# Kernel optimization log

Hardware: AMD Instinct MI355X
Metric: run time of the kernel (lower is better)

## Reference

```python
import jax, jax.numpy as jnp
import numpy as np

B, N, C, H = 4, 4096, 1024, 16
EPS = 1e-6


def setup_inputs() -> dict:
    key = jax.random.key(0)
    k1, k2, k3 = jax.random.split(key, 3)
    x = jax.random.normal(k1, (B, N, C), dtype=jnp.float32)
    qkv_w = jax.random.normal(k2, (3 * C, C), dtype=jnp.float32) * 0.02
    qkv_b = jnp.zeros((3 * C,), dtype=jnp.float32)
    proj_w = jax.random.normal(k3, (C, C), dtype=jnp.float32) * 0.02
    proj_b = jnp.zeros((C,), dtype=jnp.float32)
    return {"x": x, "qkv_w": qkv_w, "qkv_b": qkv_b, "proj_w": proj_w, "proj_b": proj_b}


def reference(x, qkv_w, qkv_b, proj_w, proj_b):
    b, n, c = x.shape
    d = c // H
    # qkv projection: (B,N,3C) -> (3,B,H,N,D)
    qkv = x @ qkv_w.T + qkv_b
    qkv = qkv.reshape(b, n, 3, H, d).transpose(2, 0, 3, 1, 4)
    q, k, v = qkv[0], qkv[1], qkv[2]
    # non-negative kernel
    q = jax.nn.sigmoid(q)
    k = jax.nn.sigmoid(k)
    # sink / source normalization (all per (B,H,N))
    k_sum = k.sum(axis=2)                                   # (B,H,D)
    sink_incoming = 1.0 / jnp.sum((q + EPS) * (k_sum[:, :, None, :] + EPS), axis=-1)
    q_sum = q.sum(axis=2)                                   # (B,H,D)
    source_outgoing = 1.0 / jnp.sum((k + EPS) * (q_sum[:, :, None, :] + EPS), axis=-1)
    k_so_sum = (k * source_outgoing[..., None]).sum(axis=2, keepdims=True)  # (B,H,1,D)
    conserved_sink = jnp.sum((q + EPS) * (k_so_sum + EPS), axis=-1) + EPS   # (B,H,N)
    q_si_sum = (q * sink_incoming[..., None]).sum(axis=2, keepdims=True)    # (B,H,1,D)
    conserved_source = jnp.sum((k + EPS) * (q_si_sum + EPS), axis=-1) + EPS # (B,H,N)
    conserved_source = jnp.clip(conserved_source, -1.0, 1.0)
    ratio = float(n) / float(n)  # q_len / k_len == 1 for self-attention
    sink_allocation = jax.nn.sigmoid(conserved_sink * ratio)               # (B,H,N)
    source_competition = jax.nn.softmax(conserved_source, axis=-1) * float(n)
    q_norm = q * sink_incoming[..., None]
    v_comp = v * source_competition[..., None]
    # linear-time attention: (B,H,D,D) then (B,H,N,D)
    kv = jnp.einsum('bhnd,bhnm->bhdm', k, v_comp)
    out = jnp.einsum('bhnd,bhdm->bhnm', q_norm, kv)
    out = out * sink_allocation[..., None]
    out = out.transpose(0, 2, 1, 3).reshape(b, n, c)
    out = out @ proj_w.T + proj_b
    # dropout is identity in eval mode
    return out
```

## Files before the change

kernel.cpp:

```cpp
#include <hip/hip_runtime.h>
#include <cstdint>
#include <cstddef>

#define EPSF 1e-6f

static constexpr int Bc  = 4;
static constexpr int Nc  = 4096;
static constexpr int Hc  = 16;
static constexpr int Dc  = 64;
static constexpr size_t HEADSZ = (size_t)64 * Nc * Dc;
static constexpr int Kd  = 1024;

typedef __attribute__((ext_vector_type(8))) short     s16x8;
typedef __attribute__((ext_vector_type(4))) float     f32x4;

__device__ __forceinline__ float sigmoid_f(float x) {
  return 1.0f / (1.0f + __expf(-x));
}

__device__ __forceinline__ unsigned short bf16_rne(float x) {
  unsigned int b = __float_as_uint(x);
  b += 0x7fffu + ((b >> 16) & 1u);
  return (unsigned short)(b >> 16);
}
__device__ __forceinline__ float bf16_to_f(unsigned short u) {
  return __uint_as_float(((unsigned int)u) << 16);
}
__device__ __forceinline__ void split_trunc(float x, unsigned short& h, unsigned short& l) {
  unsigned int b  = __float_as_uint(x);
  unsigned int hb = b & 0xffff0000u;
  h = (unsigned short)(hb >> 16);
  float res = x - __uint_as_float(hb);
  l = (unsigned short)(__float_as_uint(res) >> 16);
}

__device__ __forceinline__ void gl_lds16(const unsigned short* g, unsigned short* l) {
  __builtin_amdgcn_global_load_lds(
      (const __attribute__((address_space(1))) unsigned int*)(const void*)g,
      (__attribute__((address_space(3))) unsigned int*)(void*)l,
      16, 0, 0);
}

__global__ __launch_bounds__(256)
void split_kernel(const float* __restrict__ in, unsigned short* __restrict__ hi,
                  unsigned short* __restrict__ lo, int n4)
{
  int i = blockIdx.x * 256 + threadIdx.x;
  if (i >= n4) return;
  float4 v = ((const float4*)in)[i];
  ushort4 h, l;
  h.x = bf16_rne(v.x); l.x = bf16_rne(v.x - bf16_to_f(h.x));
  h.y = bf16_rne(v.y); l.y = bf16_rne(v.y - bf16_to_f(h.y));
  h.z = bf16_rne(v.z); l.z = bf16_rne(v.z - bf16_to_f(h.z));
  h.w = bf16_rne(v.w); l.w = bf16_rne(v.w - bf16_to_f(h.w));
  ((ushort4*)hi)[i] = h;
  ((ushort4*)lo)[i] = l;
}

template <int MODE>
__global__ __launch_bounds__(256)
void gemm_mfma(const unsigned short* __restrict__ Ah_g, const unsigned short* __restrict__ Al_g,
               const unsigned short* __restrict__ Wh_g, const unsigned short* __restrict__ Wl_g,
               const float* __restrict__ bias,
               float* __restrict__ out0, float* __restrict__ out1, float* __restrict__ out2,
               float* __restrict__ qsum_g, float* __restrict__ ksum_g)
{
  __shared__ unsigned short Ahs[128][32];
  __shared__ unsigned short Als[128][32];
  __shared__ unsigned short Whs[128][32];
  __shared__ unsigned short Wls[128][32];

  const int bid = blockIdx.x;
  const int xcd = bid & 7;
  const int idx = bid >> 3;
  int bx, by;
  if constexpr (MODE == 0) {
    bx = idx / 3;
    by = xcd * 3 + idx % 3;
  } else {
    bx = xcd * 16 + (idx >> 3);
    by = idx & 7;
  }

  const int t    = threadIdx.x;
  const int lane = t & 63;
  const int wid  = t >> 6;
  const int wr   = wid >> 1, wc = wid & 1;
  const int r16  = lane & 15, g = lane >> 4;
  const int m0   = bx * 128;
  const int r0   = by * 128;

  const int wrow = wid * 32;
  const int wl_r = lane >> 2;
  const int wl_c = (lane & 3) * 8;
  unsigned short* AhsF = &Ahs[0][0];
  unsigned short* AlsF = &Als[0][0];
  unsigned short* WhsF = &Whs[0][0];
  unsigned short* WlsF = &Wls[0][0];

  f32x4 acc[4][4];
#pragma unroll
  for (int i = 0; i < 4; ++i)
#pragma unroll
    for (int j = 0; j < 4; ++j) acc[i][j] = (f32x4){0.f, 0.f, 0.f, 0.f};

  for (int kt = 0; kt < Kd; kt += 32) {
    __syncthreads();
#pragma unroll
    for (int j = 0; j < 2; ++j) {
      const size_t ga  = (size_t)(m0 + wrow + j*16 + wl_r) * Kd + kt + wl_c;
      const size_t gw  = (size_t)(r0 + wrow + j*16 + wl_r) * Kd + kt + wl_c;
      const int    lof = wid * 1024 + j * 512;
      gl_lds16(Ah_g + ga, AhsF + lof);
      gl_lds16(Al_g + ga, AlsF + lof);
      gl_lds16(Wh_g + gw, WhsF + lof);
      gl_lds16(Wl_g + gw, WlsF + lof);
    }
    __syncthreads();

    s16x8 fah[4], fal[4], fbh[4], fbl[4];
#pragma unroll
    for (int i = 0; i < 4; ++i) {
      const int row = wr * 64 + i * 16 + r16;
      fah[i] = *(const s16x8*)&Ahs[row][g * 8];
      fal[i] = *(const s16x8*)&Als[row][g * 8];
    }
#pragma unroll
    for (int j = 0; j < 4; ++j) {
      const int row = wc * 64 + j * 16 + r16;
      fbh[j] = *(const s16x8*)&Whs[row][g * 8];
      fbl[j] = *(const s16x8*)&Wls[row][g * 8];
    }
#pragma unroll
    for (int i = 0; i < 4; ++i) {
#pragma unroll
      for (int j = 0; j < 4; ++j) {
        acc[i][j] = __builtin_amdgcn_mfma_f32_16x16x32_bf16(fah[i], fbh[j], acc[i][j], 0, 0, 0);
        acc[i][j] = __builtin_amdgcn_mfma_f32_16x16x32_bf16(fah[i], fbl[j], acc[i][j], 0, 0, 0);
        acc[i][j] = __builtin_amdgcn_mfma_f32_16x16x32_bf16(fal[i], fbh[j], acc[i][j], 0, 0, 0);
      }
    }
  }

#pragma unroll
  for (int nj = 0; nj < 4; ++nj) {
    const int colb = r0 + wc * 64 + nj * 16;
    const float bj = bias[colb + r16];
    if constexpr (MODE == 0) {
      const int tsel = colb >> 10;
      const int h    = (colb & 1023) >> 6;
      const int d    = (colb & 63) + r16;
      float* dst = (tsel == 0) ? out0 : (tsel == 1) ? out1 : out2;
      const bool sig = (tsel < 2);
      float ssum = 0.f;
#pragma unroll
      for (int mi = 0; mi < 4; ++mi) {
#pragma unroll
        for (int rg = 0; rg < 4; ++rg) {
          const int m = m0 + wr * 64 + mi * 16 + g * 4 + rg;
          float xv = acc[mi][nj][rg] + bj;
          if (sig) { xv = sigmoid_f(xv); ssum += xv; }
          const int b = m >> 12, n = m & 4095;
          dst[((size_t)(b * Hc + h) * Nc + n) * Dc + d] = xv;
        }
      }
      if (sig) {
        ssum += __shfl_xor(ssum, 16);
        ssum += __shfl_xor(ssum, 32);
        if (g == 0) {
          const int b = (m0 + wr * 64) >> 12;
          float* sdst = (tsel == 0) ? qsum_g : ksum_g;
          atomicAdd(&sdst[(b * Hc + h) * 64 + d], ssum);
        }
      }
    } else {
#pragma unroll
      for (int mi = 0; mi < 4; ++mi) {
#pragma unroll
        for (int rg = 0; rg < 4; ++rg) {
          const int m = m0 + wr * 64 + mi * 16 + g * 4 + rg;
          out0[(size_t)m * 1024 + colb + r16] = acc[mi][nj][rg] + bj;
        }
      }
    }
  }
}

__global__ __launch_bounds__(256)
void siso_kernel(const float* __restrict__ qb, const float* __restrict__ kb,
                 const float* __restrict__ q_sum, const float* __restrict__ k_sum,
                 float* __restrict__ si,
                 float* __restrict__ q_si_sum, float* __restrict__ k_so_sum)
{
  const int bh = blockIdx.x;
  const int t = threadIdx.x, lane = t & 63, w = t >> 6;
  const int c = lane & 15, r = lane >> 4;
  float4 ksd = *(const float4*)&k_sum[bh*64 + c*4];
  float4 qsd = *(const float4*)&q_sum[bh*64 + c*4];
  ksd.x += EPSF; ksd.y += EPSF; ksd.z += EPSF; ksd.w += EPSF;
  qsd.x += EPSF; qsd.y += EPSF; qsd.z += EPSF; qsd.w += EPSF;
  float4 qsi_p = {0,0,0,0}, kso_p = {0,0,0,0};
  const size_t rowbase = (size_t)bh * Nc;
  const int n00 = blockIdx.y * 256 + w * 64;
  for (int i = 0; i < 16; ++i) {
    const int n = n00 + i*4 + r;
    const size_t off = (rowbase + n) * Dc + c*4;
    float4 qv = *(const float4*)&qb[off];
    float4 kv = *(const float4*)&kb[off];
    float s1 = (qv.x+EPSF)*ksd.x + (qv.y+EPSF)*ksd.y + (qv.z+EPSF)*ksd.z + (qv.w+EPSF)*ksd.w;
    float s2 = (kv.x+EPSF)*qsd.x + (kv.y+EPSF)*qsd.y + (kv.z+EPSF)*qsd.z + (kv.w+EPSF)*qsd.w;
#pragma unroll
    for (int o = 1; o < 16; o <<= 1) {
      s1 += __shfl_xor(s1, o);
      s2 += __shfl_xor(s2, o);
    }
    const float si_n = 1.f / s1;
    const float so_n = 1.f / s2;
    if (c == 0) si[rowbase + n] = si_n;
    qsi_p.x = __builtin_fmaf(qv.x, si_n, qsi_p.x);
    qsi_p.y = __builtin_fmaf(qv.y, si_n, qsi_p.y);
    qsi_p.z = __builtin_fmaf(qv.z, si_n, qsi_p.z);
    qsi_p.w = __builtin_fmaf(qv.w, si_n, qsi_p.w);
    kso_p.x = __builtin_fmaf(kv.x, so_n, kso_p.x);
    kso_p.y = __builtin_fmaf(kv.y, so_n, kso_p.y);
    kso_p.z = __builtin_fmaf(kv.z, so_n, kso_p.z);
    kso_p.w = __builtin_fmaf(kv.w, so_n, kso_p.w);
  }
#pragma unroll
  for (int o = 16; o < 64; o <<= 1) {
    qsi_p.x += __shfl_xor(qsi_p.x, o); qsi_p.y += __shfl_xor(qsi_p.y, o);
    qsi_p.z += __shfl_xor(qsi_p.z, o); qsi_p.w += __shfl_xor(qsi_p.w, o);
    kso_p.x += __shfl_xor(kso_p.x, o); kso_p.y += __shfl_xor(kso_p.y, o);
    kso_p.z += __shfl_xor(kso_p.z, o); kso_p.w += __shfl_xor(kso_p.w, o);
  }
  __shared__ float red[2][4][64];
  if (r == 0) {
    *(float4*)&red[0][w][c*4] = qsi_p;
    *(float4*)&red[1][w][c*4] = kso_p;
  }
  __syncthreads();
  if (t < 64) {
    atomicAdd(&q_si_sum[bh*64 + t], red[0][0][t]+red[0][1][t]+red[0][2][t]+red[0][3][t]);
  } else if (t < 128) {
    const int l = t - 64;
    atomicAdd(&k_so_sum[bh*64 + l], red[1][0][l]+red[1][1][l]+red[1][2][l]+red[1][3][l]);
  }
}

__global__ __launch_bounds__(256)
void conserved_kernel(const float* __restrict__ qb, const float* __restrict__ kb,
                      const float* __restrict__ q_si_sum, const float* __restrict__ k_so_sum,
                      const float* __restrict__ si,
                      float* __restrict__ qscale, float* __restrict__ sc_raw,
                      float* __restrict__ exp_sum)
{
  const int bh = blockIdx.x;
  const int t = threadIdx.x, lane = t & 63, w = t >> 6;
  const int c = lane & 15, r = lane >> 4;
  float4 ksod = *(const float4*)&k_so_sum[bh*64 + c*4];
  float4 qsid = *(const float4*)&q_si_sum[bh*64 + c*4];
  ksod.x += EPSF; ksod.y += EPSF; ksod.z += EPSF; ksod.w += EPSF;
  qsid.x += EPSF; qsid.y += EPSF; qsid.z += EPSF; qsid.w += EPSF;
  float ep = 0.f;
  const size_t rowbase = (size_t)bh * Nc;
  const int n00 = blockIdx.y * 256 + w * 64;
  for (int i = 0; i < 16; ++i) {
    const int n = n00 + i*4 + r;
    const size_t off = (rowbase + n) * Dc + c*4;
    float4 qv = *(const float4*)&qb[off];
    float4 kv = *(const float4*)&kb[off];
    float s1 = (qv.x+EPSF)*ksod.x + (qv.y+EPSF)*ksod.y + (qv.z+EPSF)*ksod.z + (qv.w+EPSF)*ksod.w;
    float s2 = (kv.x+EPSF)*qsid.x + (kv.y+EPSF)*qsid.y + (kv.z+EPSF)*qsid.z + (kv.w+EPSF)*qsid.w;
#pragma unroll
    for (int o = 1; o < 16; o <<= 1) {
      s1 += __shfl_xor(s1, o);
      s2 += __shfl_xor(s2, o);
    }
    if (c == 0) {
      const float sa = sigmoid_f(s1 + EPSF);
      float cs = s2 + EPSF;
      cs = fminf(fmaxf(cs, -1.f), 1.f);
      const float e = __expf(cs);
      qscale[rowbase + n] = sa * si[rowbase + n];
      sc_raw[rowbase + n] = e;
      ep += e;
    }
  }
  ep += __shfl_xor(ep, 16);
  ep += __shfl_xor(ep, 32);
  __shared__ float red[4];
  if (lane == 0) red[w] = ep;
  __syncthreads();
  if (t == 0) atomicAdd(&exp_sum[bh], red[0]+red[1]+red[2]+red[3]);
}

__global__ __launch_bounds__(256)
void kv_kernel(const float* __restrict__ kb, const float* __restrict__ vb,
               const float* __restrict__ sc_raw, const float* __restrict__ exp_sum,
               float* __restrict__ kvout)
{
  const int bh = blockIdx.x, ch = blockIdx.y;
  const int t = threadIdx.x;
  const int m = t & 63, dg = t >> 6;
  const float scl = (float)Nc / exp_sum[bh];
  __shared__ float ks[64][64];
  __shared__ float vs[64][64];
  float acc[16];
#pragma unroll
  for (int i = 0; i < 16; ++i) acc[i] = 0.f;

  for (int c0 = ch*256; c0 < ch*256 + 256; c0 += 64) {
    __syncthreads();
#pragma unroll
    for (int j = 0; j < 4; ++j) {
      const int f = t + 256*j;
      const int row = f >> 4, cb = (f & 15) * 4;
      const size_t gidx = ((size_t)bh*Nc + c0 + row) * Dc + cb;
      *(float4*)&ks[row][cb] = *(const float4*)&kb[gidx];
      float4 vv = *(const float4*)&vb[gidx];
      const float s = sc_raw[(size_t)bh*Nc + c0 + row] * scl;
      vv.x *= s; vv.y *= s; vv.z *= s; vv.w *= s;
      *(float4*)&vs[row][cb] = vv;
    }
    __syncthreads();
#pragma unroll 8
    for (int n = 0; n < 64; ++n) {
      const float vv = vs[n][m];
#pragma unroll
      for (int dd = 0; dd < 4; ++dd) {
        float4 kk = *(const float4*)&ks[n][dg*16 + dd*4];
        acc[dd*4+0] = __builtin_fmaf(kk.x, vv, acc[dd*4+0]);
        acc[dd*4+1] = __builtin_fmaf(kk.y, vv, acc[dd*4+1]);
        acc[dd*4+2] = __builtin_fmaf(kk.z, vv, acc[dd*4+2]);
        acc[dd*4+3] = __builtin_fmaf(kk.w, vv, acc[dd*4+3]);
      }
    }
  }
#pragma unroll
  for (int dd = 0; dd < 16; ++dd)
    atomicAdd(&kvout[(size_t)bh*4096 + (size_t)(dg*16 + dd)*64 + m], acc[dd]);
}

__global__ __launch_bounds__(256)
void out_kernel(const float* __restrict__ qb, const float* __restrict__ kvin,
                const float* __restrict__ qscale,
                unsigned short* __restrict__ attn_h, unsigned short* __restrict__ attn_l)
{
  const int bh = blockIdx.x, cy = blockIdx.y;
  const int t = threadIdx.x;
  const int c0 = cy * 64;
  __shared__ float kvs[64][68];
  __shared__ float qT[64][68];
  __shared__ float qsc[64];

#pragma unroll
  for (int j = 0; j < 4; ++j) {
    const int f = t + 256*j;
    const int d = f >> 4, cb = (f & 15) * 4;
    *(float4*)&kvs[d][cb] = *(const float4*)&kvin[(size_t)bh*4096 + (size_t)d*64 + cb];
  }
#pragma unroll
  for (int j = 0; j < 4; ++j) {
    const int f = t + 256*j;
    const int n = f >> 4, db = (f & 15) * 4;
    float4 qv = *(const float4*)&qb[((size_t)bh*Nc + c0 + n) * Dc + db];
    qT[db+0][n] = qv.x; qT[db+1][n] = qv.y; qT[db+2][n] = qv.z; qT[db+3][n] = qv.w;
  }
  if (t < 16) *(float4*)&qsc[t*4] = *(const float4*)&qscale[(size_t)bh*Nc + c0 + t*4];
  __syncthreads();

  const int ng = t & 15, mg = t >> 4;
  float acc[4][4];
#pragma unroll
  for (int i = 0; i < 4; ++i)
#pragma unroll
    for (int j = 0; j < 4; ++j) acc[i][j] = 0.f;

#pragma unroll 16
  for (int d = 0; d < 64; ++d) {
    float4 a = *(const float4*)&qT[d][ng*4];
    float4 b = *(const float4*)&kvs[d][mg*4];
    float av[4] = {a.x,a.y,a.z,a.w};
    float bv[4] = {b.x,b.y,b.z,b.w};
#pragma unroll
    for (int i = 0; i < 4; ++i)
#pragma unroll
      for (int j = 0; j < 4; ++j)
        acc[i][j] = __builtin_fmaf(av[i], bv[j], acc[i][j]);
  }

  const int b = bh >> 4, h = bh & 15;
#pragma unroll
  for (int i = 0; i < 4; ++i) {
    const int n = c0 + ng*4 + i;
    const float s = qsc[ng*4 + i];
    const size_t base = ((size_t)b * Nc + n) * 1024 + h * Dc + mg * 4;
    ushort4 hh, ll;
    float v0 = acc[i][0]*s, v1 = acc[i][1]*s, v2 = acc[i][2]*s, v3 = acc[i][3]*s;
    split_trunc(v0, hh.x, ll.x);
    split_trunc(v1, hh.y, ll.y);
    split_trunc(v2, hh.z, ll.z);
    split_trunc(v3, hh.w, ll.w);
    *(ushort4*)&attn_h[base] = hh;
    *(ushort4*)&attn_l[base] = ll;
  }
}

extern "C" void kernel_launch(void* const* d_in, const int* in_sizes, int n_in,
                              void* d_out, int out_size, void* d_ws, size_t ws_size,
                              hipStream_t stream)
{
  const float* x      = (const float*)d_in[0];
  const float* qkv_w  = (const float*)d_in[1];
  const float* qkv_b  = (const float*)d_in[2];
  const float* proj_w = (const float*)d_in[3];
  const float* proj_b = (const float*)d_in[4];
  float* out = (float*)d_out;
  float* ws  = (float*)d_ws;

  float* qb = ws;
  float* kb = ws + HEADSZ;
  float* vb = ws + 2*HEADSZ;
  unsigned short* attn_h = (unsigned short*)vb;
  unsigned short* attn_l = attn_h + HEADSZ;

  float* sm      = ws + 3*HEADSZ;
  float* q_sum   = sm;
  float* k_sum   = sm + 4096;
  float* q_si    = sm + 8192;
  float* k_so    = sm + 12288;
  float* exp_sum = sm + 16384;
  float* si      = sm + 20480;
  float* qscale  = si + 262144;
  float* sc_raw  = qscale + 262144;
  float* kvbuf   = sc_raw + 262144;

  unsigned short* Wh = (unsigned short*)(kvbuf + 262144);
  unsigned short* Wl = Wh + 3145728;
  unsigned short* Ph = Wl + 3145728;
  unsigned short* Pl = Ph + 1048576;

  unsigned short* xh = (unsigned short*)d_out;
  unsigned short* xl = xh + 16777216;

  hipMemsetAsync(sm, 0, 20480 * sizeof(float), stream);
  hipMemsetAsync(kvbuf, 0, 262144 * sizeof(float), stream);

  split_kernel<<<16384, 256, 0, stream>>>(x, xh, xl, 4194304);
  split_kernel<<<3072, 256, 0, stream>>>(qkv_w, Wh, Wl, 786432);
  split_kernel<<<1024, 256, 0, stream>>>(proj_w, Ph, Pl, 262144);

  gemm_mfma<0><<<3072, 256, 0, stream>>>(xh, xl, Wh, Wl, qkv_b,
                                         qb, kb, vb, q_sum, k_sum);

  siso_kernel<<<dim3(64, 16), 256, 0, stream>>>(qb, kb, q_sum, k_sum, si, q_si, k_so);
  conserved_kernel<<<dim3(64, 16), 256, 0, stream>>>(qb, kb, q_si, k_so, si, qscale, sc_raw, exp_sum);
  kv_kernel<<<dim3(64, 16), 256, 0, stream>>>(kb, vb, sc_raw, exp_sum, kvbuf);
  out_kernel<<<dim3(64, 64), 256, 0, stream>>>(qb, kvbuf, qscale, attn_h, attn_l);

  gemm_mfma<1><<<1024, 256, 0, stream>>>(attn_h, attn_l, Ph, Pl, proj_b,
                                         out, nullptr, nullptr, nullptr, nullptr);
}
```

Baseline: 704.9 us.

## Triple-buffer GEMM LDS with swizzle and 256-row tiles over 512 threads

The split-bf16 GEMM kernel now uses 8 waves per block with 256x128 output tiles and a three-stage LDS ring buffer. Global-to-LDS loads for future k-tiles are issued while MFMAs run on the current tile, and each stage waits only on outstanding vmcnt before a barrier. The LDS layout gains an XOR swizzle to cut bank conflicts, and MFMA sections raise wave priority. This targets the load latency and double barrier per k-step of the old loop, at the cost of more LDS (about 144KB) and fewer blocks per CU. The epilogue must now map 8 waves onto the taller tile correctly.

```diff
diff --git a/kernel.cpp b/kernel.cpp
--- a/kernel.cpp
+++ b/kernel.cpp
@@ -10,6 +10,7 @@
 static constexpr int Dc  = 64;
 static constexpr size_t HEADSZ = (size_t)64 * Nc * Dc;
 static constexpr int Kd  = 1024;
+static constexpr int BUFSH = 24576;
 
 typedef __attribute__((ext_vector_type(8))) short     s16x8;
 typedef __attribute__((ext_vector_type(4))) float     f32x4;
@@ -57,29 +58,93 @@
   ((ushort4*)lo)[i] = l;
 }
 
+__device__ __forceinline__ void gstage(unsigned short* __restrict__ dst,
+                                       const unsigned short* __restrict__ Ah_g,
+                                       const unsigned short* __restrict__ Al_g,
+                                       const unsigned short* __restrict__ Wh_g,
+                                       const unsigned short* __restrict__ Wl_g,
+                                       int m0, int r0, int kt, int wid, int lane)
+{
+  const int lr = lane >> 2;
+  const int sw = ((lane & 3) ^ ((lr >> 1) & 3)) * 8;
+  const size_t g0 = (size_t)(m0 + wid*32 + lr) * Kd + kt + sw;
+  const size_t g1 = g0 + (size_t)16 * Kd;
+  unsigned short* d0 = dst + wid*1024;
+  gl_lds16(Ah_g + g0, d0);
+  gl_lds16(Ah_g + g1, d0 + 512);
+  gl_lds16(Al_g + g0, d0 + 8192);
+  gl_lds16(Al_g + g1, d0 + 8704);
+  const size_t gw = (size_t)(r0 + wid*16 + lr) * Kd + kt + sw;
+  unsigned short* d1 = dst + 16384 + wid*512;
+  gl_lds16(Wh_g + gw, d1);
+  gl_lds16(Wl_g + gw, d1 + 4096);
+}
+
+__device__ __forceinline__ void gstep(const unsigned short* __restrict__ base,
+                                      int wr, int wc, int r16, int g,
+                                      f32x4 (&acc)[4][4])
+{
+  const unsigned short* Ah_s = base;
+  const unsigned short* Al_s = base + 8192;
+  const unsigned short* Wh_s = base + 16384;
+  const unsigned short* Wl_s = base + 20480;
+  const int gsw = (g ^ ((r16 >> 1) & 3)) * 8;
+  s16x8 fbh[4], fbl[4];
+#pragma unroll
+  for (int j = 0; j < 4; ++j) {
+    const int off = (wc*64 + j*16 + r16)*32 + gsw;
+    fbh[j] = *(const s16x8*)&Wh_s[off];
+    fbl[j] = *(const s16x8*)&Wl_s[off];
+  }
+#pragma unroll
+  for (int ph = 0; ph < 2; ++ph) {
+    s16x8 fah[2], fal[2];
+#pragma unroll
+    for (int ii = 0; ii < 2; ++ii) {
+      const int off = (wr*64 + (ph*2+ii)*16 + r16)*32 + gsw;
+      fah[ii] = *(const s16x8*)&Ah_s[off];
+      fal[ii] = *(const s16x8*)&Al_s[off];
+    }
+    __builtin_amdgcn_s_setprio(1);
+#pragma unroll
+    for (int pr = 0; pr < 3; ++pr)
+#pragma unroll
+      for (int ii = 0; ii < 2; ++ii)
+#pragma unroll
+        for (int j = 0; j < 4; ++j)
+          acc[ph*2+ii][j] = __builtin_amdgcn_mfma_f32_16x16x32_bf16(
+              (pr == 2) ? fal[ii] : fah[ii],
+              (pr == 1) ? fbl[j]  : fbh[j],
+              acc[ph*2+ii][j], 0, 0, 0);
+    __builtin_amdgcn_s_setprio(0);
+  }
+}
+
+#define WAIT_BAR(N) do { \
+  asm volatile("s_waitcnt vmcnt(" #N ")" ::: "memory"); \
+  __builtin_amdgcn_s_barrier(); \
+} while (0)
+
 template <int MODE>
-__global__ __launch_bounds__(256)
+__global__ __launch_bounds__(512)
 void gemm_mfma(const unsigned short* __restrict__ Ah_g, const unsigned short* __restrict__ Al_g,
                const unsigned short* __restrict__ Wh_g, const unsigned short* __restrict__ Wl_g,
                const float* __restrict__ bias,
                float* __restrict__ out0, float* __restrict__ out1, float* __restrict__ out2,
                float* __restrict__ qsum_g, float* __restrict__ ksum_g)
 {
-  __shared__ unsigned short Ahs[128][32];
-  __shared__ unsigned short Als[128][32];
-  __shared__ unsigned short Whs[128][32];
-  __shared__ unsigned short Wls[128][32];
+  __shared__ unsigned short lds[3 * BUFSH];
 
   const int bid = blockIdx.x;
   const int xcd = bid & 7;
   const int idx = bid >> 3;
   int bx, by;
   if constexpr (MODE == 0) {
+    by = xcd * 3 + idx % 3;
     bx = idx / 3;
-    by = xcd * 3 + idx % 3;
   } else {
-    bx = xcd * 16 + (idx >> 3);
-    by = idx & 7;
+    by = xcd;
+    bx = idx;
   }
 
   const int t    = threadIdx.x;
@@ -87,60 +152,36 @@
   const int wid  = t >> 6;
   const int wr   = wid >> 1, wc = wid & 1;
   const int r16  = lane & 15, g = lane >> 4;
-  const int m0   = bx * 128;
+  const int m0   = bx * 256;
   const int r0   = by * 128;
 
-  const int wrow = wid * 32;
-  const int wl_r = lane >> 2;
-  const int wl_c = (lane & 3) * 8;
-  unsigned short* AhsF = &Ahs[0][0];
-  unsigned short* AlsF = &Als[0][0];
-  unsigned short* WhsF = &Whs[0][0];
-  unsigned short* WlsF = &Wls[0][0];
-
   f32x4 acc[4][4];
 #pragma unroll
   for (int i = 0; i < 4; ++i)
 #pragma unroll
     for (int j = 0; j < 4; ++j) acc[i][j] = (f32x4){0.f, 0.f, 0.f, 0.f};
 
-  for (int kt = 0; kt < Kd; kt += 32) {
-    __syncthreads();
-#pragma unroll
-    for (int j = 0; j < 2; ++j) {
-      const size_t ga  = (size_t)(m0 + wrow + j*16 + wl_r) * Kd + kt + wl_c;
-      const size_t gw  = (size_t)(r0 + wrow + j*16 + wl_r) * Kd + kt + wl_c;
-      const int    lof = wid * 1024 + j * 512;
-      gl_lds16(Ah_g + ga, AhsF + lof);
-      gl_lds16(Al_g + ga, AlsF + lof);
-      gl_lds16(Wh_g + gw, WhsF + lof);
-      gl_lds16(Wl_g + gw, WlsF + lof);
-    }
-    __syncthreads();
-
-    s16x8 fah[4], fal[4], fbh[4], fbl[4];
-#pragma unroll
-    for (int i = 0; i < 4; ++i) {
-      const int row = wr * 64 + i * 16 + r16;
-      fah[i] = *(const s16x8*)&Ahs[row][g * 8];
-      fal[i] = *(const s16x8*)&Als[row][g * 8];
-    }
-#pragma unroll
-    for (int j = 0; j < 4; ++j) {
-      const int row = wc * 64 + j * 16 + r16;
-      fbh[j] = *(const s16x8*)&Whs[row][g * 8];
-      fbl[j] = *(const s16x8*)&Wls[row][g * 8];
-    }
-#pragma unroll
-    for (int i = 0; i < 4; ++i) {
-#pragma unroll
-      for (int j = 0; j < 4; ++j) {
-        acc[i][j] = __builtin_amdgcn_mfma_f32_16x16x32_bf16(fah[i], fbh[j], acc[i][j], 0, 0, 0);
-        acc[i][j] = __builtin_amdgcn_mfma_f32_16x16x32_bf16(fah[i], fbl[j], acc[i][j], 0, 0, 0);
-        acc[i][j] = __builtin_amdgcn_mfma_f32_16x16x32_bf16(fal[i], fbh[j], acc[i][j], 0, 0, 0);
-      }
-    }
-  }
+  unsigned short* L = &lds[0];
+
+  gstage(L,          Ah_g, Al_g, Wh_g, Wl_g, m0, r0, 0,  wid, lane);
+  gstage(L + BUFSH,  Ah_g, Al_g, Wh_g, Wl_g, m0, r0, 32, wid, lane);
+  WAIT_BAR(6);
+
+  for (int tt = 0; tt < 30; tt += 3) {
+    const int kb = tt * 32;
+    gstage(L + 2*BUFSH, Ah_g, Al_g, Wh_g, Wl_g, m0, r0, kb + 64,  wid, lane);
+    gstep(L,           wr, wc, r16, g, acc);
+    WAIT_BAR(6);
+    gstage(L,           Ah_g, Al_g, Wh_g, Wl_g, m0, r0, kb + 96,  wid, lane);
+    gstep(L + BUFSH,   wr, wc, r16, g, acc);
+    WAIT_BAR(6);
+    gstage(L + BUFSH,   Ah_g, Al_g, Wh_g, Wl_g, m0, r0, kb + 128, wid, lane);
+    gstep(L + 2*BUFSH, wr, wc, r16, g, acc);
+    WAIT_BAR(6);
+  }
+  gstep(L, wr, wc, r16, g, acc);
+  WAIT_BAR(0);
+  gstep(L + BUFSH, wr, wc, r16, g, acc);
 
 #pragma unroll
   for (int nj = 0; nj < 4; ++nj) {
@@ -450,7 +491,7 @@
   split_kernel<<<3072, 256, 0, stream>>>(qkv_w, Wh, Wl, 786432);
   split_kernel<<<1024, 256, 0, stream>>>(proj_w, Ph, Pl, 262144);
 
-  gemm_mfma<0><<<3072, 256, 0, stream>>>(xh, xl, Wh, Wl, qkv_b,
+  gemm_mfma<0><<<1536, 512, 0, stream>>>(xh, xl, Wh, Wl, qkv_b,
                                          qb, kb, vb, q_sum, k_sum);
 
   siso_kernel<<<dim3(64, 16), 256, 0, stream>>>(qb, kb, q_sum, k_sum, si, q_si, k_so);
@@ -458,6 +499,6 @@
   kv_kernel<<<dim3(64, 16), 256, 0, stream>>>(kb, vb, sc_raw, exp_sum, kvbuf);
   out_kernel<<<dim3(64, 64), 256, 0, stream>>>(qb, kvbuf, qscale, attn_h, attn_l);
 
-  gemm_mfma<1><<<1024, 256, 0, stream>>>(attn_h, attn_l, Ph, Pl, proj_b,
-                                         out, nullptr, nullptr, nullptr, nullptr);
-}
+  gemm_mfma<1><<<512, 512, 0, stream>>>(attn_h, attn_l, Ph, Pl, proj_b,
+                                        out, nullptr, nullptr, nullptr, nullptr);
+}
```

Result: faster. 683.8 us (-3.0%).
